# Optimization experiments

Hardware: AMD Instinct MI355X
Metric: run time of the kernel (lower is better)

The kernel has to match this reference:

```python
import jax, jax.numpy as jnp
import numpy as np

N = 20000          # nodes
E = 320000         # edges
D_IN = 128         # input_dim
HGC = 64           # hidden per gconv layer
LG = 4             # number of ChebConv layers
K = 4              # Chebyshev order (hardcoded)
NUM_CLASSES = 2
HID_BYS = 16       # bayesian hidden_dim (hardcoded)
NSAMP = 25         # 5 outer x 5 inner chained sampling iterations
BN_SCALE = 1.0 / np.sqrt(1.0 + 1e-5)  # eval BatchNorm with default running stats
COS_EPS = 1e-8


def setup_inputs() -> dict:
    key = jax.random.key(0)
    ks = jax.random.split(key, 16)
    f32 = jnp.float32
    d = {}
    d["features"] = jax.random.normal(ks[0], (N, D_IN), f32)
    d["edge_index"] = jax.random.randint(ks[1], (2, E), 0, N)
    d["edgenet_input"] = jax.random.normal(ks[2], (E, 128), f32)
    half = 64  # edgenet_input_dim // 2
    # associationP MLP: Linear(64,512) ReLU BN Linear(512,256) ReLU BN Drop Linear(256,128)
    d["We1"] = jax.random.normal(ks[3], (512, half), f32) * np.sqrt(2.0 / half)
    d["be1"] = jnp.zeros((512,), f32)
    d["We2"] = jax.random.normal(ks[4], (256, 512), f32) * np.sqrt(2.0 / 512)
    d["be2"] = jnp.zeros((256,), f32)
    d["We3"] = jax.random.normal(ks[5], (128, 256), f32) * np.sqrt(2.0 / 256)
    d["be3"] = jnp.zeros((128,), f32)
    # ChebConv weights, [K, in, out], no bias
    d["cheb_w0"] = jax.random.normal(ks[6], (K, D_IN, HGC), f32) * np.sqrt(2.0 / D_IN)
    d["cheb_w1"] = jax.random.normal(ks[7], (K, HGC, HGC), f32) * np.sqrt(2.0 / HGC)
    d["cheb_w2"] = jax.random.normal(ks[8], (K, HGC, HGC), f32) * np.sqrt(2.0 / HGC)
    d["cheb_w3"] = jax.random.normal(ks[9], (K, HGC, HGC), f32) * np.sqrt(2.0 / HGC)
    cls_in = HGC * LG  # 256, jumping-knowledge concat
    d["Wm1"] = jax.random.normal(ks[10], (256, cls_in), f32) * np.sqrt(2.0 / cls_in)
    d["bm1"] = jnp.zeros((256,), f32)
    d["Wm2"] = jax.random.normal(ks[11], (NUM_CLASSES, 256), f32) * np.sqrt(2.0 / 256)
    d["bm2"] = jnp.zeros((NUM_CLASSES,), f32)
    d["Wl"] = jax.random.normal(ks[12], (HID_BYS, D_IN), f32) * np.sqrt(2.0 / D_IN)
    d["bl"] = jnp.zeros((HID_BYS,), f32)
    hl_in = NSAMP * HID_BYS  # 400, the freshly-created Linear2
    d["Whl"] = jax.random.normal(ks[13], (NUM_CLASSES, hl_in), f32) * np.sqrt(1.0 / hl_in)
    d["bhl"] = jnp.zeros((NUM_CLASSES,), f32)
    # prior Normal(0,1) samples, one per node per sampling iteration
    d["noise"] = jax.random.normal(ks[14], (NSAMP, N, HID_BYS), f32)
    return d


def _edge_mlp(x, We1, be1, We2, be2, We3, be3):
    h = jax.nn.relu(x @ We1.T + be1) * BN_SCALE
    h = jax.nn.relu(h @ We2.T + be2) * BN_SCALE
    return h @ We3.T + be3


def _forward(features, edge_index, edgenet_input, We1, be1, We2, be2, We3, be3,
             cheb_w0, cheb_w1, cheb_w2, cheb_w3, Wm1, bm1, Wm2, bm2,
             Wl, bl, Whl, bhl, noise):
    row, col = edge_index[0], edge_index[1]

    # ---- edge weights via associationP (cosine similarity head) ----
    h1 = _edge_mlp(edgenet_input[:, :64], We1, be1, We2, be2, We3, be3)
    h2 = _edge_mlp(edgenet_input[:, 64:], We1, be1, We2, be2, We3, be3)
    n1 = jnp.maximum(jnp.sqrt(jnp.sum(h1 * h1, -1)), COS_EPS)
    n2 = jnp.maximum(jnp.sqrt(jnp.sum(h2 * h2, -1)), COS_EPS)
    cos = jnp.sum(h1 * h2, -1) / (n1 * n2)
    ew = (cos + 1.0) * 0.5  # [E]

    # ---- ChebConv sym-normalized scaled Laplacian (lambda_max=2 -> zero diag) ----
    w = jnp.where(row == col, 0.0, ew)  # remove_self_loops
    deg = jax.ops.segment_sum(w, row, num_segments=N)
    dinv = jnp.where(deg > 0, jax.lax.rsqrt(deg), 0.0)
    lapw = -dinv[row] * w * dinv[col]  # L_hat off-diagonal weights

    def prop(x):  # L_hat @ x  (diag is exactly 0)
        return jax.ops.segment_sum(lapw[:, None] * x[row], col, num_segments=N)

    def cheb(x, W):  # W: [K, in, out]
        tx0, tx1 = x, prop(x)
        out = tx0 @ W[0] + tx1 @ W[1]
        for k in range(2, K):
            tx2 = 2.0 * prop(tx1) - tx0
            out = out + tx2 @ W[k]
            tx0, tx1 = tx1, tx2
        return out

    # ---- dense_gcn branch with jumping-knowledge concat ----
    h = jax.nn.relu(cheb(features, cheb_w0))
    jk = h
    for W in (cheb_w1, cheb_w2, cheb_w3):
        h = jax.nn.relu(cheb(h, W))
        jk = jnp.concatenate([jk, h], axis=1)
    m = jax.nn.relu(jk @ Wm1.T + bm1) * BN_SCALE
    logit1 = m @ Wm2.T + bm2  # [N, C]

    # ---- bys_gcn branch: 25 chained iterations h <- noise + scatter_add(w*h[src]) ----
    h0 = features @ Wl.T + bl  # [N, 16]

    def step(hc, nz):
        agg = jax.ops.segment_sum(ew[:, None] * hc[row], col, num_segments=N)
        hn = nz + agg
        return hn, hn

    _, states = jax.lax.scan(step, h0, noise)  # [25, N, 16]
    # faithful to torch .view(N, -1) on the [5,5,N,16] stack (row-major reshape)
    feats2 = states.reshape(N, NSAMP * HID_BYS)  # [N, 400]
    logit2 = jax.nn.sigmoid(feats2 @ Whl.T + bhl)  # [N, C]

    p1 = jax.nn.softmax(logit1, axis=1)
    p2 = jax.nn.softmax(logit2, axis=1)
    return p1, p2, jnp.maximum(p1, p2)


def reference(features, edge_index, edgenet_input, We1, be1, We2, be2, We3, be3,
              cheb_w0, cheb_w1, cheb_w2, cheb_w3, Wm1, bm1, Wm2, bm2,
              Wl, bl, Whl, bhl, noise):
    return _forward(features, edge_index, edgenet_input, We1, be1, We2, be2, We3, be3,
                    cheb_w0, cheb_w1, cheb_w2, cheb_w3, Wm1, bm1, Wm2, bm2,
                    Wl, bl, Whl, bhl, noise)
```

## Files before the change

kernel.cpp:

```cpp
#include <hip/hip_runtime.h>
#include <math.h>

#define NN 20000
#define EE 320000
#define BN_SC 0.9999950000374997f

typedef __attribute__((ext_vector_type(8))) short bf16x8;
typedef __attribute__((ext_vector_type(4))) float f32x4;

__device__ __forceinline__ unsigned short f2b(float x) {
  unsigned int u = __builtin_bit_cast(unsigned int, x);
  u += 0x7FFFu + ((u >> 16) & 1u);
  return (unsigned short)(u >> 16);
}
__device__ __forceinline__ void split2(float x, unsigned short& h, unsigned short& l) {
  h = f2b(x);
  float hf = __builtin_bit_cast(float, (unsigned int)h << 16);
  l = f2b(x - hf);
}

__global__ __launch_bounds__(256) void k_wpack(const float* __restrict__ W, unsigned short* __restrict__ Wh,
                                               unsigned short* __restrict__ Wl, int C, int K) {
  int i = blockIdx.x * 256 + threadIdx.x;
  if (i >= C * K) return;
  int e = i & 7;
  int lane = (i >> 3) & 63;
  int tile = i >> 9;
  int KT = K >> 5;
  int kt = tile % KT, ct = tile / KT;
  int lr = lane & 15, lg = lane >> 4;
  int col = ct * 16 + lr;
  int k = kt * 32 + lg * 8 + e;
  unsigned short h, l;
  split2(W[(size_t)col * K + k], h, l);
  Wh[i] = h;
  Wl[i] = l;
}

__global__ __launch_bounds__(256) void k_count(const int* __restrict__ colv, int* __restrict__ cnt) {
  int e = blockIdx.x * 256 + threadIdx.x;
  if (e < EE) atomicAdd(&cnt[colv[e]], 1);
}

__global__ __launch_bounds__(1024) void k_scan(const int* __restrict__ cnt, int* __restrict__ offs) {
  __shared__ int sb[1024];
  __shared__ int sc;
  int t = threadIdx.x;
  if (t == 0) { sc = 0; offs[0] = 0; }
  __syncthreads();
  for (int base = 0; base < NN; base += 1024) {
    int v = (base + t < NN) ? cnt[base + t] : 0;
    sb[t] = v;
    __syncthreads();
    for (int off = 1; off < 1024; off <<= 1) {
      int x = (t >= off) ? sb[t - off] : 0;
      __syncthreads();
      sb[t] += x;
      __syncthreads();
    }
    if (base + t < NN) offs[base + t + 1] = sc + sb[t];
    __syncthreads();
    if (t == 0) sc += sb[1023];
    __syncthreads();
  }
}

__global__ __launch_bounds__(256) void k_fill(const int* __restrict__ colv, const int* __restrict__ offs,
                                              int* __restrict__ cur, int* __restrict__ eid) {
  int e = blockIdx.x * 256 + threadIdx.x;
  if (e < EE) {
    int d = colv[e];
    int p = atomicAdd(&cur[d], 1);
    eid[offs[d] + p] = e;
  }
}

__global__ __launch_bounds__(256) void k_sort(const int* __restrict__ offs, int* __restrict__ eid) {
  int n = blockIdx.x * 256 + threadIdx.x;
  if (n >= NN) return;
  int j0 = offs[n], j1 = offs[n + 1];
  for (int i = j0 + 1; i < j1; ++i) {
    int v = eid[i];
    int j = i - 1;
    while (j >= j0 && eid[j] > v) { eid[j + 1] = eid[j]; --j; }
    eid[j + 1] = v;
  }
}

__global__ __launch_bounds__(256) void k_pack(const int* __restrict__ eid, const int* __restrict__ rowi,
                                              const int* __restrict__ colv,
                                              const float* __restrict__ ew, const float* __restrict__ dinv,
                                              float2* __restrict__ packW, float2* __restrict__ packL) {
  int j = blockIdx.x * 256 + threadIdx.x;
  if (j < EE) {
    int e = eid[j];
    int r = rowi[e], c = colv[e];
    float rw = __int_as_float(r);
    float w = (r == c) ? 0.f : ew[e];
    packW[j] = make_float2(ew[e], rw);
    packL[j] = make_float2(-dinv[r] * w * dinv[c], rw);
  }
}

#define MFMA16(a, b, c) __builtin_amdgcn_mfma_f32_16x16x32_bf16(a, b, c, 0, 0, 0)

__global__ __launch_bounds__(512, 2) void k_edge_mlp(
    const float* __restrict__ X,
    const unsigned short* __restrict__ W1h, const unsigned short* __restrict__ W1l, const float* __restrict__ b1,
    const unsigned short* __restrict__ W2h, const unsigned short* __restrict__ W2l, const float* __restrict__ b2,
    const unsigned short* __restrict__ W3h, const unsigned short* __restrict__ W3l, const float* __restrict__ b3,
    float* __restrict__ ew) {
  __shared__ __align__(16) unsigned short POOL[24576];
  unsigned short* Xh = POOL;
  unsigned short* Xl = POOL + 4096;
  unsigned short* H2ch = POOL + 8192;
  unsigned short* H2cl = POOL + 16384;
  float* H3 = (float*)(POOL + 8192);

  const int tid = threadIdx.x;
  const int wv = tid >> 6;
  const int lane = tid & 63;
  const int lr = lane & 15;
  const int lg = lane >> 4;
  const int e0 = blockIdx.x * 32;
  const int lane8 = lane << 3;

  const int rt1 = wv & 3;
  const int ch1 = wv >> 2;

  {
    int row = tid >> 3, eighth = tid & 7;
    const float* src = X + (size_t)(e0 + (row >> 1)) * 128 + (row & 1) * 64 + eighth * 8;
    float4 a = ((const float4*)src)[0];
    float4 b = ((const float4*)src)[1];
    float vals[8] = {a.x, a.y, a.z, a.w, b.x, b.y, b.z, b.w};
    unsigned short hs[8], ls[8];
#pragma unroll
    for (int j = 0; j < 8; ++j) split2(vals[j], hs[j], ls[j]);
    int chunk = eighth ^ (row & 7);
    int idxs = row * 64 + chunk * 8;
#pragma unroll
    for (int j = 0; j < 8; ++j) { Xh[idxs + j] = hs[j]; Xl[idxs + j] = ls[j]; }
  }
  __syncthreads();

  auto l1_compute = [&](int c, int b) {
    unsigned short* H1h = POOL + 8192 + b * 8192;
    unsigned short* H1l = POOL + 12288 + b * 8192;
    f32x4 acc1[2];
#pragma unroll
    for (int cti = 0; cti < 2; ++cti) acc1[cti] = f32x4{0.f, 0.f, 0.f, 0.f};
#pragma unroll
    for (int kt = 0; kt < 2; ++kt) {
      int arow = 16 * rt1 + lr;
      int aidx = arow * 64 + ((4 * kt + lg) ^ (arow & 7)) * 8;
      bf16x8 ah = *(const bf16x8*)&Xh[aidx];
      bf16x8 al = *(const bf16x8*)&Xl[aidx];
#pragma unroll
      for (int cti = 0; cti < 2; ++cti) {
        int off = (((4 * c + 2 * ch1 + cti) * 2 + kt) << 9) + lane8;
        bf16x8 bh = *(const bf16x8*)(W1h + off);
        bf16x8 bl = *(const bf16x8*)(W1l + off);
        acc1[cti] = MFMA16(ah, bh, acc1[cti]);
        acc1[cti] = MFMA16(ah, bl, acc1[cti]);
        acc1[cti] = MFMA16(al, bh, acc1[cti]);
      }
    }
#pragma unroll
    for (int cti = 0; cti < 2; ++cti) {
      int colL = 16 * (2 * ch1 + cti) + lr;
      float bias = b1[64 * c + colL];
#pragma unroll
      for (int r = 0; r < 4; ++r) {
        float v = fmaxf(acc1[cti][r] + bias, 0.f) * BN_SC;
        unsigned short hs, ls;
        split2(v, hs, ls);
        int row = 16 * rt1 + 4 * lg + r;
        int idxs = row * 64 + (((colL >> 3) ^ (row & 7)) * 8) + (colL & 7);
        H1h[idxs] = hs;
        H1l[idxs] = ls;
      }
    }
  };

  f32x4 acc2[4][2];
#pragma unroll
  for (int rt = 0; rt < 4; ++rt)
#pragma unroll
    for (int ct = 0; ct < 2; ++ct) acc2[rt][ct] = f32x4{0.f, 0.f, 0.f, 0.f};

  l1_compute(0, 0);
  __syncthreads();

  for (int kc = 0; kc < 8; ++kc) {
    int cur = kc & 1;
    unsigned short* H1h = POOL + 8192 + cur * 8192;
    unsigned short* H1l = POOL + 12288 + cur * 8192;
    bf16x8 p2h[2], p2l[2];
    {
#pragma unroll
      for (int ct = 0; ct < 2; ++ct) {
        int off = (((8 * ct + wv) * 16 + 2 * kc) << 9) + lane8;
        p2h[ct] = *(const bf16x8*)(W2h + off);
        p2l[ct] = *(const bf16x8*)(W2l + off);
      }
    }
    if (kc < 7) l1_compute(kc + 1, cur ^ 1);
    bf16x8 q2h[2], q2l[2];
    {
#pragma unroll
      for (int ct = 0; ct < 2; ++ct) {
        int off = (((8 * ct + wv) * 16 + 2 * kc + 1) << 9) + lane8;
        q2h[ct] = *(const bf16x8*)(W2h + off);
        q2l[ct] = *(const bf16x8*)(W2l + off);
      }
    }
#pragma unroll
    for (int rtg = 0; rtg < 2; ++rtg) {
      bf16x8 ah[2], al[2];
#pragma unroll
      for (int rti = 0; rti < 2; ++rti) {
        int arow = 32 * rtg + 16 * rti + lr;
        int aidx = arow * 64 + (lg ^ (arow & 7)) * 8;
        ah[rti] = *(const bf16x8*)&H1h[aidx];
        al[rti] = *(const bf16x8*)&H1l[aidx];
      }
#pragma unroll
      for (int ct = 0; ct < 2; ++ct)
#pragma unroll
        for (int rti = 0; rti < 2; ++rti) {
          acc2[2 * rtg + rti][ct] = MFMA16(ah[rti], p2h[ct], acc2[2 * rtg + rti][ct]);
          acc2[2 * rtg + rti][ct] = MFMA16(ah[rti], p2l[ct], acc2[2 * rtg + rti][ct]);
          acc2[2 * rtg + rti][ct] = MFMA16(al[rti], p2h[ct], acc2[2 * rtg + rti][ct]);
        }
    }
#pragma unroll
    for (int rtg = 0; rtg < 2; ++rtg) {
      bf16x8 ah[2], al[2];
#pragma unroll
      for (int rti = 0; rti < 2; ++rti) {
        int arow = 32 * rtg + 16 * rti + lr;
        int aidx = arow * 64 + ((4 + lg) ^ (arow & 7)) * 8;
        ah[rti] = *(const bf16x8*)&H1h[aidx];
        al[rti] = *(const bf16x8*)&H1l[aidx];
      }
#pragma unroll
      for (int ct = 0; ct < 2; ++ct)
#pragma unroll
        for (int rti = 0; rti < 2; ++rti) {
          acc2[2 * rtg + rti][ct] = MFMA16(ah[rti], q2h[ct], acc2[2 * rtg + rti][ct]);
          acc2[2 * rtg + rti][ct] = MFMA16(ah[rti], q2l[ct], acc2[2 * rtg + rti][ct]);
          acc2[2 * rtg + rti][ct] = MFMA16(al[rti], q2h[ct], acc2[2 * rtg + rti][ct]);
        }
    }
    __syncthreads();
  }

  f32x4 acc3[4];
#pragma unroll
  for (int rt = 0; rt < 4; ++rt) acc3[rt] = f32x4{0.f, 0.f, 0.f, 0.f};
  const int w3col = 16 * wv + lr;

#pragma unroll
  for (int ch = 0; ch < 2; ++ch) {
    bf16x8 w3h_c, w3l_c;
    {
      int off = ((wv * 8 + 4 * ch) << 9) + lane8;
      w3h_c = *(const bf16x8*)(W3h + off);
      w3l_c = *(const bf16x8*)(W3l + off);
    }
    if (ch) __syncthreads();
    {
      int colC = 16 * wv + lr;
      float bias = b2[128 * ch + colC];
#pragma unroll
      for (int rt = 0; rt < 4; ++rt) {
#pragma unroll
        for (int r = 0; r < 4; ++r) {
          float v = fmaxf(acc2[rt][ch][r] + bias, 0.f) * BN_SC;
          unsigned short hs, ls;
          split2(v, hs, ls);
          int row = 16 * rt + 4 * lg + r;
          int idxs = row * 128 + (((colC >> 3) ^ (row & 7)) * 8) + (colC & 7);
          H2ch[idxs] = hs;
          H2cl[idxs] = ls;
        }
      }
    }
    __syncthreads();
#pragma unroll
    for (int kt = 0; kt < 4; ++kt) {
      bf16x8 w3h_n, w3l_n;
      if (kt < 3) {
        int off = ((wv * 8 + 4 * ch + kt + 1) << 9) + lane8;
        w3h_n = *(const bf16x8*)(W3h + off);
        w3l_n = *(const bf16x8*)(W3l + off);
      }
#pragma unroll
      for (int rtg = 0; rtg < 2; ++rtg) {
        bf16x8 ah[2], al[2];
#pragma unroll
        for (int rti = 0; rti < 2; ++rti) {
          int arow = 32 * rtg + 16 * rti + lr;
          int aidx = arow * 128 + (((4 * kt + lg) ^ (arow & 7)) * 8);
          ah[rti] = *(const bf16x8*)&H2ch[aidx];
          al[rti] = *(const bf16x8*)&H2cl[aidx];
        }
#pragma unroll
        for (int rti = 0; rti < 2; ++rti) {
          acc3[2 * rtg + rti] = MFMA16(ah[rti], w3h_c, acc3[2 * rtg + rti]);
          acc3[2 * rtg + rti] = MFMA16(ah[rti], w3l_c, acc3[2 * rtg + rti]);
          acc3[2 * rtg + rti] = MFMA16(al[rti], w3h_c, acc3[2 * rtg + rti]);
        }
      }
      w3h_c = w3h_n;
      w3l_c = w3l_n;
    }
  }
  __syncthreads();

  {
    float bias = b3[w3col];
#pragma unroll
    for (int rt = 0; rt < 4; ++rt)
#pragma unroll
      for (int r = 0; r < 4; ++r)
        H3[(16 * rt + 4 * lg + r) * 128 + w3col] = acc3[rt][r] + bias;
  }
  __syncthreads();

  {
    int i = tid >> 4, j = tid & 15;
    const float* ra = &H3[(2 * i) * 128];
    const float* rb = &H3[(2 * i + 1) * 128];
    float dot = 0.f, s1 = 0.f, s2 = 0.f;
#pragma unroll
    for (int s = 0; s < 8; ++s) {
      float a = ra[j + 16 * s], b = rb[j + 16 * s];
      dot += a * b;
      s1 += a * a;
      s2 += b * b;
    }
#pragma unroll
    for (int m = 8; m >= 1; m >>= 1) {
      dot += __shfl_xor(dot, m);
      s1 += __shfl_xor(s1, m);
      s2 += __shfl_xor(s2, m);
    }
    if (j == 0) {
      float n1 = fmaxf(sqrtf(s1), 1e-8f);
      float n2 = fmaxf(sqrtf(s2), 1e-8f);
      float cosv = dot / (n1 * n2);
      ew[e0 + i] = (cosv + 1.f) * 0.5f;
    }
  }
}

__global__ __launch_bounds__(256) void k_deg(const int* __restrict__ rowi, const int* __restrict__ colv,
                                             const float* __restrict__ ew, float* __restrict__ deg) {
  int e = blockIdx.x * 256 + threadIdx.x;
  if (e < EE) {
    int r = rowi[e];
    float w = (r == colv[e]) ? 0.f : ew[e];
    atomicAdd(&deg[r], w);
  }
}
__global__ __launch_bounds__(256) void k_dinv(const float* __restrict__ deg, float* __restrict__ dinv) {
  int n = blockIdx.x * 256 + threadIdx.x;
  if (n < NN) { float d = deg[n]; dinv[n] = d > 0.f ? 1.f / sqrtf(d) : 0.f; }
}

template <int DIM>
__global__ __launch_bounds__(256) void k_prop(const float* __restrict__ x, int ldx,
                                              const float* __restrict__ y, int ldy,
                                              float alpha, float beta,
                                              float* __restrict__ outv, int ldo,
                                              const float2* __restrict__ packL,
                                              const int* __restrict__ offs) {
  constexpr int FG = DIM / 4;
  int idx = blockIdx.x * 256 + threadIdx.x;
  int n = idx / FG, g = (idx % FG) * 4;
  if (n >= NN) return;
  float ax = 0.f, ay = 0.f, az = 0.f, aw = 0.f;
  int j1 = offs[n + 1];
  for (int j = offs[n]; j < j1; ++j) {
    float2 p = packL[j];
    float4 v = *(const float4*)(x + (size_t)__float_as_int(p.y) * ldx + g);
    ax += p.x * v.x; ay += p.x * v.y; az += p.x * v.z; aw += p.x * v.w;
  }
  float4 r = make_float4(alpha * ax, alpha * ay, alpha * az, alpha * aw);
  if (beta != 0.f) {
    float4 yv = *(const float4*)(y + (size_t)n * ldy + g);
    r.x += beta * yv.x; r.y += beta * yv.y; r.z += beta * yv.z; r.w += beta * yv.w;
  }
  *(float4*)(outv + (size_t)n * ldo + g) = r;
}

template <int DK>
__global__ __launch_bounds__(512) void k_combine(const float* __restrict__ t0, int ld0,
                                                 const float* __restrict__ t1, int ld1,
                                                 const float* __restrict__ t2, int ld2,
                                                 const float* __restrict__ t3, int ld3,
                                                 const float* __restrict__ W,
                                                 float* __restrict__ outp) {
  int n = blockIdx.x * 8 + (threadIdx.x >> 6);
  int c = threadIdx.x & 63;
  if (n >= NN) return;
  const float* r0 = t0 + (size_t)n * ld0;
  const float* r1 = t1 + (size_t)n * ld1;
  const float* r2 = t2 + (size_t)n * ld2;
  const float* r3 = t3 + (size_t)n * ld3;
  const float* w0 = W;
  const float* w1 = W + DK * 64;
  const float* w2 = W + 2 * DK * 64;
  const float* w3 = W + 3 * DK * 64;
  float acc = 0.f;
#pragma unroll 4
  for (int d = 0; d < DK; ++d) {
    acc += r0[d] * w0[d * 64 + c];
    acc += r1[d] * w1[d * 64 + c];
    acc += r2[d] * w2[d * 64 + c];
    acc += r3[d] * w3[d * 64 + c];
  }
  outp[(size_t)n * 256 + c] = fmaxf(acc, 0.f);
}

__global__ void k_tr256(const float* __restrict__ A, float* __restrict__ At) {
  int c = blockIdx.x, k = threadIdx.x;
  At[(size_t)k * 256 + c] = A[(size_t)c * 256 + k];
}

__global__ __launch_bounds__(256) void k_mlogit(const float* __restrict__ jk, const float* __restrict__ Wm1t,
                                                const float* __restrict__ bm1, const float* __restrict__ Wm2,
                                                const float* __restrict__ bm2, float* __restrict__ logit1) {
  __shared__ float jks[16 * 256];
  __shared__ float red[16 * 8];
  int tid = threadIdx.x, n0 = blockIdx.x * 16;
  {
    const float4* src = (const float4*)(jk + (size_t)n0 * 256);
    float4* dst = (float4*)jks;
#pragma unroll
    for (int u = 0; u < 4; ++u) dst[tid + 256 * u] = src[tid + 256 * u];
  }
  __syncthreads();
  int c = tid;
  float acc[16];
  float bb = bm1[c];
#pragma unroll
  for (int r = 0; r < 16; ++r) acc[r] = bb;
  for (int k = 0; k < 256; k += 4) {
    float w0 = Wm1t[(size_t)(k + 0) * 256 + c];
    float w1 = Wm1t[(size_t)(k + 1) * 256 + c];
    float w2 = Wm1t[(size_t)(k + 2) * 256 + c];
    float w3 = Wm1t[(size_t)(k + 3) * 256 + c];
#pragma unroll
    for (int r = 0; r < 16; ++r) {
      float4 jv = *(const float4*)&jks[r * 256 + k];
      acc[r] += jv.x * w0 + jv.y * w1 + jv.z * w2 + jv.w * w3;
    }
  }
  float w20 = Wm2[c], w21 = Wm2[256 + c];
  int wid = tid >> 6, lane = tid & 63;
#pragma unroll
  for (int r = 0; r < 16; ++r) {
    float mv = fmaxf(acc[r], 0.f) * BN_SC;
    float v0 = mv * w20, v1 = mv * w21;
#pragma unroll
    for (int m = 32; m >= 1; m >>= 1) {
      v0 += __shfl_xor(v0, m, 64);
      v1 += __shfl_xor(v1, m, 64);
    }
    if (lane == 0) { red[r * 8 + wid] = v0; red[r * 8 + 4 + wid] = v1; }
  }
  __syncthreads();
  if (tid < 32) {
    int r = tid >> 1, cls = tid & 1;
    float s = red[r * 8 + cls * 4] + red[r * 8 + cls * 4 + 1] + red[r * 8 + cls * 4 + 2] + red[r * 8 + cls * 4 + 3];
    logit1[(size_t)(n0 + r) * 2 + cls] = s + bm2[cls];
  }
}

__global__ __launch_bounds__(256) void k_h0(const float* __restrict__ feat, const float* __restrict__ Wl,
                                            const float* __restrict__ bl, float* __restrict__ h0) {
  int idx = blockIdx.x * 256 + threadIdx.x;
  if (idx >= NN * 16) return;
  int n = idx >> 4, j = idx & 15;
  const float* fr = feat + (size_t)n * 128;
  const float* wr = Wl + (size_t)j * 128;
  float acc = bl[j];
#pragma unroll 8
  for (int d = 0; d < 128; d += 4) {
    float4 f = *(const float4*)(fr + d);
    float4 w = *(const float4*)(wr + d);
    acc += f.x * w.x + f.y * w.y + f.z * w.z + f.w * w.w;
  }
  h0[idx] = acc;
}

__global__ __launch_bounds__(256) void k_bys(const float* __restrict__ hprev, const float* __restrict__ nz,
                                             float* __restrict__ hout,
                                             const float2* __restrict__ packW,
                                             const int* __restrict__ offs) {
  int idx = blockIdx.x * 256 + threadIdx.x;
  int n = idx >> 2, g = (idx & 3) * 4;
  if (n >= NN) return;
  float ax = 0.f, ay = 0.f, az = 0.f, aw = 0.f;
  int j1 = offs[n + 1];
  for (int j = offs[n]; j < j1; ++j) {
    float2 p = packW[j];
    float4 v = *(const float4*)(hprev + ((size_t)__float_as_int(p.y) << 4) + g);
    ax += p.x * v.x; ay += p.x * v.y; az += p.x * v.z; aw += p.x * v.w;
  }
  float4 nv = *(const float4*)(nz + ((size_t)n << 4) + g);
  *(float4*)(hout + ((size_t)n << 4) + g) = make_float4(nv.x + ax, nv.y + ay, nv.z + az, nv.w + aw);
}

__global__ __launch_bounds__(256) void k_final(const float* __restrict__ states, const float* __restrict__ Whl,
                                               const float* __restrict__ bhl, const float* __restrict__ logit1,
                                               float* __restrict__ outp) {
  int n = blockIdx.x * 4 + (threadIdx.x >> 6);
  int l = threadIdx.x & 63;
  if (n >= NN) return;
  const float* sf = states + (size_t)n * 400;
  float a0 = 0.f, a1 = 0.f;
  for (int t = l; t < 400; t += 64) {
    float v = sf[t];
    a0 += v * Whl[t];
    a1 += v * Whl[400 + t];
  }
#pragma unroll
  for (int m = 32; m >= 1; m >>= 1) {
    a0 += __shfl_xor(a0, m, 64);
    a1 += __shfl_xor(a1, m, 64);
  }
  if (l == 0) {
    float z0 = 1.f / (1.f + expf(-(a0 + bhl[0])));
    float z1 = 1.f / (1.f + expf(-(a1 + bhl[1])));
    float p20 = 1.f / (1.f + expf(z1 - z0));
    float p21 = 1.f - p20;
    float l10 = logit1[(size_t)n * 2], l11 = logit1[(size_t)n * 2 + 1];
    float p10 = 1.f / (1.f + expf(l11 - l10));
    float p11 = 1.f - p10;
    outp[(size_t)n * 2] = p10;
    outp[(size_t)n * 2 + 1] = p11;
    outp[2 * NN + (size_t)n * 2] = p20;
    outp[2 * NN + (size_t)n * 2 + 1] = p21;
    outp[4 * NN + (size_t)n * 2] = fmaxf(p10, p20);
    outp[4 * NN + (size_t)n * 2 + 1] = fmaxf(p11, p21);
  }
}

extern "C" void kernel_launch(void* const* d_in, const int* in_sizes, int n_in,
                              void* d_out, int out_size, void* d_ws, size_t ws_size,
                              hipStream_t stream) {
  const float* feat = (const float*)d_in[0];
  const int* ei = (const int*)d_in[1];
  const float* xen = (const float*)d_in[2];
  const float* We1 = (const float*)d_in[3];
  const float* be1 = (const float*)d_in[4];
  const float* We2 = (const float*)d_in[5];
  const float* be2 = (const float*)d_in[6];
  const float* We3 = (const float*)d_in[7];
  const float* be3 = (const float*)d_in[8];
  const float* cw[4] = {(const float*)d_in[9], (const float*)d_in[10], (const float*)d_in[11], (const float*)d_in[12]};
  const float* Wm1 = (const float*)d_in[13];
  const float* bm1 = (const float*)d_in[14];
  const float* Wm2 = (const float*)d_in[15];
  const float* bm2 = (const float*)d_in[16];
  const float* Wl = (const float*)d_in[17];
  const float* bl = (const float*)d_in[18];
  const float* Whl = (const float*)d_in[19];
  const float* bhl = (const float*)d_in[20];
  const float* noise = (const float*)d_in[21];
  float* outp = (float*)d_out;

  char* wp_ = (char*)d_ws;
  auto alloc = [&](size_t bytes) {
    char* p = wp_;
    wp_ += (bytes + 255) & ~(size_t)255;
    return p;
  };
  float* ew = (float*)alloc((size_t)EE * 4);
  float* deg = (float*)alloc((size_t)NN * 4);
  float* dinv = (float*)alloc((size_t)NN * 4);
  int* cnt = (int*)alloc((size_t)NN * 4);
  int* offs = (int*)alloc((size_t)(NN + 1) * 4);
  int* eid = (int*)alloc((size_t)EE * 4);
  float2* packW = (float2*)alloc((size_t)EE * 8);
  float2* packL = (float2*)alloc((size_t)EE * 8);
  float* tx1 = (float*)alloc((size_t)NN * 128 * 4);
  float* tx2 = (float*)alloc((size_t)NN * 128 * 4);
  float* tx3 = (float*)alloc((size_t)NN * 128 * 4);
  float* jk = (float*)alloc((size_t)NN * 256 * 4);
  float* logit1 = (float*)alloc((size_t)NN * 2 * 4);
  float* Wm1t = (float*)alloc((size_t)256 * 256 * 4);
  float* h0 = (float*)alloc((size_t)NN * 16 * 4);
  float* states = (float*)alloc((size_t)25 * NN * 16 * 4);
  unsigned short* W1h = (unsigned short*)alloc((size_t)32768 * 2);
  unsigned short* W1l = (unsigned short*)alloc((size_t)32768 * 2);
  unsigned short* W2h = (unsigned short*)alloc((size_t)131072 * 2);
  unsigned short* W2l = (unsigned short*)alloc((size_t)131072 * 2);
  unsigned short* W3h = (unsigned short*)alloc((size_t)32768 * 2);
  unsigned short* W3l = (unsigned short*)alloc((size_t)32768 * 2);

  const int* rowi = ei;
  const int* colv = ei + EE;

  k_wpack<<<128, 256, 0, stream>>>(We1, W1h, W1l, 512, 64);
  k_wpack<<<512, 256, 0, stream>>>(We2, W2h, W2l, 256, 512);
  k_wpack<<<128, 256, 0, stream>>>(We3, W3h, W3l, 128, 256);

  hipMemsetAsync(cnt, 0, (size_t)NN * 4, stream);
  hipMemsetAsync(deg, 0, (size_t)NN * 4, stream);
  k_count<<<1250, 256, 0, stream>>>(colv, cnt);
  k_scan<<<1, 1024, 0, stream>>>(cnt, offs);
  hipMemsetAsync(cnt, 0, (size_t)NN * 4, stream);
  k_fill<<<1250, 256, 0, stream>>>(colv, offs, cnt, eid);
  k_sort<<<79, 256, 0, stream>>>(offs, eid);

  k_edge_mlp<<<10000, 512, 0, stream>>>(xen, W1h, W1l, be1, W2h, W2l, be2, W3h, W3l, be3, ew);

  k_deg<<<1250, 256, 0, stream>>>(rowi, colv, ew, deg);
  k_dinv<<<79, 256, 0, stream>>>(deg, dinv);
  k_pack<<<1250, 256, 0, stream>>>(eid, rowi, colv, ew, dinv, packW, packL);
  k_tr256<<<256, 256, 0, stream>>>(Wm1, Wm1t);

  k_prop<128><<<2500, 256, 0, stream>>>(feat, 128, feat, 128, 1.f, 0.f, tx1, 128, packL, offs);
  k_prop<128><<<2500, 256, 0, stream>>>(tx1, 128, feat, 128, 2.f, -1.f, tx2, 128, packL, offs);
  k_prop<128><<<2500, 256, 0, stream>>>(tx2, 128, tx1, 128, 2.f, -1.f, tx3, 128, packL, offs);
  k_combine<128><<<2500, 512, 0, stream>>>(feat, 128, tx1, 128, tx2, 128, tx3, 128, cw[0], jk);
  for (int l = 1; l < 4; ++l) {
    const float* xin = jk + (l - 1) * 64;
    k_prop<64><<<1250, 256, 0, stream>>>(xin, 256, xin, 256, 1.f, 0.f, tx1, 64, packL, offs);
    k_prop<64><<<1250, 256, 0, stream>>>(tx1, 64, xin, 256, 2.f, -1.f, tx2, 64, packL, offs);
    k_prop<64><<<1250, 256, 0, stream>>>(tx2, 64, tx1, 64, 2.f, -1.f, tx3, 64, packL, offs);
    k_combine<64><<<2500, 512, 0, stream>>>(xin, 256, tx1, 64, tx2, 64, tx3, 64, cw[l], jk + l * 64);
  }
  k_mlogit<<<1250, 256, 0, stream>>>(jk, Wm1t, bm1, Wm2, bm2, logit1);

  k_h0<<<1250, 256, 0, stream>>>(feat, Wl, bl, h0);
  const float* hprev = h0;
  for (int s = 0; s < 25; ++s) {
    float* hout = states + (size_t)s * NN * 16;
    k_bys<<<313, 256, 0, stream>>>(hprev, noise + (size_t)s * NN * 16, hout, packW, offs);
    hprev = hout;
  }
  k_final<<<5000, 256, 0, stream>>>(states, Whl, bhl, logit1, outp);
}
```

Measured before the change: 1.863 ms.

## Parallelize CSR scan, sort adjacency in LDS, pack bf16 splits with cvt_pk

Replaces the single-block sequential prefix scan with a three-kernel multi-block scan. Moves the per-node insertion sort into shared memory, one node per thread across more blocks, so it no longer shuffles global memory. Uses v_cvt_pk_bf16_f32 to split fp32 values into hi/lo bf16 pairs two at a time, with vectorized LDS stores in the edge MLP. These target serial preprocessing latency and conversion ALU cost, at the price of two extra kernel launches and higher LDS use in the sort kernel.

```diff
diff --git a/kernel.cpp b/kernel.cpp
--- a/kernel.cpp
+++ b/kernel.cpp
@@ -17,6 +17,18 @@
   h = f2b(x);
   float hf = __builtin_bit_cast(float, (unsigned int)h << 16);
   l = f2b(x - hf);
+}
+
+__device__ __forceinline__ unsigned int cvtpk(float a, float b) {
+  unsigned int r;
+  asm("v_cvt_pk_bf16_f32 %0, %1, %2" : "=v"(r) : "v"(a), "v"(b));
+  return r;
+}
+__device__ __forceinline__ void split_pair(float x0, float x1, unsigned int& hp, unsigned int& lp) {
+  hp = cvtpk(x0, x1);
+  float h0 = __builtin_bit_cast(float, hp << 16);
+  float h1 = __builtin_bit_cast(float, hp & 0xFFFF0000u);
+  lp = cvtpk(x0 - h0, x1 - h1);
 }
 
 __global__ __launch_bounds__(256) void k_wpack(const float* __restrict__ W, unsigned short* __restrict__ Wh,
@@ -42,27 +54,40 @@
   if (e < EE) atomicAdd(&cnt[colv[e]], 1);
 }
 
-__global__ __launch_bounds__(1024) void k_scan(const int* __restrict__ cnt, int* __restrict__ offs) {
-  __shared__ int sb[1024];
-  __shared__ int sc;
+__global__ __launch_bounds__(256) void k_scan1(const int* __restrict__ cnt, int* __restrict__ offs,
+                                               int* __restrict__ bsum) {
+  __shared__ int sb[256];
+  int t = threadIdx.x, i = blockIdx.x * 256 + t;
+  int v = (i < NN) ? cnt[i] : 0;
+  sb[t] = v;
+  __syncthreads();
+  for (int off = 1; off < 256; off <<= 1) {
+    int x = (t >= off) ? sb[t - off] : 0;
+    __syncthreads();
+    sb[t] += x;
+    __syncthreads();
+  }
+  if (i < NN) offs[i + 1] = sb[t];
+  if (t == 255) bsum[blockIdx.x] = sb[255];
+}
+__global__ __launch_bounds__(128) void k_scan2(int* __restrict__ bsum) {
+  __shared__ int sb[128];
   int t = threadIdx.x;
-  if (t == 0) { sc = 0; offs[0] = 0; }
+  int v = (t < 79) ? bsum[t] : 0;
+  sb[t] = v;
   __syncthreads();
-  for (int base = 0; base < NN; base += 1024) {
-    int v = (base + t < NN) ? cnt[base + t] : 0;
-    sb[t] = v;
+  for (int off = 1; off < 128; off <<= 1) {
+    int x = (t >= off) ? sb[t - off] : 0;
     __syncthreads();
-    for (int off = 1; off < 1024; off <<= 1) {
-      int x = (t >= off) ? sb[t - off] : 0;
-      __syncthreads();
-      sb[t] += x;
-      __syncthreads();
-    }
-    if (base + t < NN) offs[base + t + 1] = sc + sb[t];
+    sb[t] += x;
     __syncthreads();
-    if (t == 0) sc += sb[1023];
-    __syncthreads();
-  }
+  }
+  if (t < 79) bsum[t] = sb[t] - v;
+}
+__global__ __launch_bounds__(256) void k_scan3(const int* __restrict__ bsum, int* __restrict__ offs) {
+  int i = blockIdx.x * 256 + threadIdx.x;
+  if (i == 0) offs[0] = 0;
+  if (i < NN) offs[i + 1] += bsum[blockIdx.x];
 }
 
 __global__ __launch_bounds__(256) void k_fill(const int* __restrict__ colv, const int* __restrict__ offs,
@@ -75,15 +100,28 @@
   }
 }
 
-__global__ __launch_bounds__(256) void k_sort(const int* __restrict__ offs, int* __restrict__ eid) {
-  int n = blockIdx.x * 256 + threadIdx.x;
+__global__ __launch_bounds__(64) void k_sortl(const int* __restrict__ offs, int* __restrict__ eid) {
+  __shared__ int buf[64 * 97];
+  int n = blockIdx.x * 64 + threadIdx.x;
   if (n >= NN) return;
-  int j0 = offs[n], j1 = offs[n + 1];
-  for (int i = j0 + 1; i < j1; ++i) {
-    int v = eid[i];
-    int j = i - 1;
-    while (j >= j0 && eid[j] > v) { eid[j + 1] = eid[j]; --j; }
-    eid[j + 1] = v;
+  int j0 = offs[n], j1 = offs[n + 1], d = j1 - j0;
+  int* b = &buf[threadIdx.x * 97];
+  if (d <= 96) {
+    for (int i = 0; i < d; ++i) b[i] = eid[j0 + i];
+    for (int i = 1; i < d; ++i) {
+      int v = b[i];
+      int j = i - 1;
+      while (j >= 0 && b[j] > v) { b[j + 1] = b[j]; --j; }
+      b[j + 1] = v;
+    }
+    for (int i = 0; i < d; ++i) eid[j0 + i] = b[i];
+  } else {
+    for (int i = j0 + 1; i < j1; ++i) {
+      int v = eid[i];
+      int j = i - 1;
+      while (j >= j0 && eid[j] > v) { eid[j + 1] = eid[j]; --j; }
+      eid[j + 1] = v;
+    }
   }
 }
 
@@ -134,13 +172,13 @@
     float4 a = ((const float4*)src)[0];
     float4 b = ((const float4*)src)[1];
     float vals[8] = {a.x, a.y, a.z, a.w, b.x, b.y, b.z, b.w};
-    unsigned short hs[8], ls[8];
-#pragma unroll
-    for (int j = 0; j < 8; ++j) split2(vals[j], hs[j], ls[j]);
+    unsigned int hp[4], lp[4];
+#pragma unroll
+    for (int p = 0; p < 4; ++p) split_pair(vals[2 * p], vals[2 * p + 1], hp[p], lp[p]);
     int chunk = eighth ^ (row & 7);
     int idxs = row * 64 + chunk * 8;
-#pragma unroll
-    for (int j = 0; j < 8; ++j) { Xh[idxs + j] = hs[j]; Xl[idxs + j] = ls[j]; }
+    *(uint4*)&Xh[idxs] = make_uint4(hp[0], hp[1], hp[2], hp[3]);
+    *(uint4*)&Xl[idxs] = make_uint4(lp[0], lp[1], lp[2], lp[3]);
   }
   __syncthreads();
 
@@ -170,15 +208,22 @@
     for (int cti = 0; cti < 2; ++cti) {
       int colL = 16 * (2 * ch1 + cti) + lr;
       float bias = b1[64 * c + colL];
+      float vv[4];
+#pragma unroll
+      for (int r = 0; r < 4; ++r) vv[r] = fmaxf(acc1[cti][r] + bias, 0.f) * BN_SC;
+      unsigned int hp0, lp0, hp1, lp1;
+      split_pair(vv[0], vv[1], hp0, lp0);
+      split_pair(vv[2], vv[3], hp1, lp1);
+      unsigned short hs[4] = {(unsigned short)hp0, (unsigned short)(hp0 >> 16),
+                              (unsigned short)hp1, (unsigned short)(hp1 >> 16)};
+      unsigned short ls[4] = {(unsigned short)lp0, (unsigned short)(lp0 >> 16),
+                              (unsigned short)lp1, (unsigned short)(lp1 >> 16)};
 #pragma unroll
       for (int r = 0; r < 4; ++r) {
-        float v = fmaxf(acc1[cti][r] + bias, 0.f) * BN_SC;
-        unsigned short hs, ls;
-        split2(v, hs, ls);
         int row = 16 * rt1 + 4 * lg + r;
         int idxs = row * 64 + (((colL >> 3) ^ (row & 7)) * 8) + (colL & 7);
-        H1h[idxs] = hs;
-        H1l[idxs] = ls;
+        H1h[idxs] = hs[r];
+        H1l[idxs] = ls[r];
       }
     }
   };
@@ -275,15 +320,22 @@
       float bias = b2[128 * ch + colC];
 #pragma unroll
       for (int rt = 0; rt < 4; ++rt) {
+        float vv[4];
+#pragma unroll
+        for (int r = 0; r < 4; ++r) vv[r] = fmaxf(acc2[rt][ch][r] + bias, 0.f) * BN_SC;
+        unsigned int hp0, lp0, hp1, lp1;
+        split_pair(vv[0], vv[1], hp0, lp0);
+        split_pair(vv[2], vv[3], hp1, lp1);
+        unsigned short hs[4] = {(unsigned short)hp0, (unsigned short)(hp0 >> 16),
+                                (unsigned short)hp1, (unsigned short)(hp1 >> 16)};
+        unsigned short ls[4] = {(unsigned short)lp0, (unsigned short)(lp0 >> 16),
+                                (unsigned short)lp1, (unsigned short)(lp1 >> 16)};
 #pragma unroll
         for (int r = 0; r < 4; ++r) {
-          float v = fmaxf(acc2[rt][ch][r] + bias, 0.f) * BN_SC;
-          unsigned short hs, ls;
-          split2(v, hs, ls);
           int row = 16 * rt + 4 * lg + r;
           int idxs = row * 128 + (((colC >> 3) ^ (row & 7)) * 8) + (colC & 7);
-          H2ch[idxs] = hs;
-          H2cl[idxs] = ls;
+          H2ch[idxs] = hs[r];
+          H2cl[idxs] = ls[r];
         }
       }
     }
@@ -585,6 +637,7 @@
   float* dinv = (float*)alloc((size_t)NN * 4);
   int* cnt = (int*)alloc((size_t)NN * 4);
   int* offs = (int*)alloc((size_t)(NN + 1) * 4);
+  int* bsum = (int*)alloc((size_t)128 * 4);
   int* eid = (int*)alloc((size_t)EE * 4);
   float2* packW = (float2*)alloc((size_t)EE * 8);
   float2* packL = (float2*)alloc((size_t)EE * 8);
@@ -613,10 +666,12 @@
   hipMemsetAsync(cnt, 0, (size_t)NN * 4, stream);
   hipMemsetAsync(deg, 0, (size_t)NN * 4, stream);
   k_count<<<1250, 256, 0, stream>>>(colv, cnt);
-  k_scan<<<1, 1024, 0, stream>>>(cnt, offs);
+  k_scan1<<<79, 256, 0, stream>>>(cnt, offs, bsum);
+  k_scan2<<<1, 128, 0, stream>>>(bsum);
+  k_scan3<<<79, 256, 0, stream>>>(bsum, offs);
   hipMemsetAsync(cnt, 0, (size_t)NN * 4, stream);
   k_fill<<<1250, 256, 0, stream>>>(colv, offs, cnt, eid);
-  k_sort<<<79, 256, 0, stream>>>(offs, eid);
+  k_sortl<<<313, 64, 0, stream>>>(offs, eid);
 
   k_edge_mlp<<<10000, 512, 0, stream>>>(xen, W1h, W1l, be1, W2h, W2l, be2, W3h, W3l, be3, ew);
 
```

Result: slower. 2.007 ms (+7.7%).
